# Kernel tuning notes

Measured on AMD Instinct MI355X. Metric: run time of the kernel, lower is better.

The kernel has to match this reference:

```python
import jax, jax.numpy as jnp
import numpy as np

D = 128          # embed_features
N = 4096         # cells per batch
M = 8192         # genes / regions
FB1, FB2, FR, FA = 100, 100, 256, 512


def setup_inputs() -> dict:
    key = jax.random.key(0)
    ks = jax.random.split(key, 16)
    s = 0.05  # weight scale to keep activations in a sane range
    return {
        "u1": jax.random.normal(ks[0], (N, FB1), jnp.float32),
        "u2": jax.random.normal(ks[1], (N, FB2), jnp.float32),
        "v1": jax.random.normal(ks[2], (M, FR), jnp.float32),
        "v2": jax.random.normal(ks[3], (M, FA), jnp.float32),
        # linear layers stored as [in, out] so y = x @ W
        "Wb1": jax.random.normal(ks[4], (FB1, D), jnp.float32) * s,
        "Wb2": jax.random.normal(ks[5], (FB2, D), jnp.float32) * s,
        "Wrna1": jax.random.normal(ks[6], (FR, 2 * D), jnp.float32) * s,
        "Wrna2": jax.random.normal(ks[7], (2 * D, D), jnp.float32) * s,
        "gene_act": jax.random.normal(ks[8], (FA, FR), jnp.float32) * s,
        "w_prod1": jax.random.normal(ks[9], (D,), jnp.float32),
        "w_add1": jax.random.normal(ks[10], (2 * D,), jnp.float32),
        "w_prod2": jax.random.normal(ks[11], (D,), jnp.float32),
        "w_add2": jax.random.normal(ks[12], (2 * D,), jnp.float32),
        "bias_1": jax.random.normal(ks[13], (), jnp.float32),
        "bias_2": jax.random.normal(ks[14], (), jnp.float32),
    }


def _pair_scores(eu, ev, w_prod, w_add, bias):
    # Algebraically identical to the original all-pairs form:
    #   (eu[:,None,:] * ev[None,:,:]) @ w_prod  ==  (eu * w_prod) @ ev.T
    #   cat(eu, ev) @ w_add  ==  eu @ w_add[:D]  +  ev @ w_add[D:]
    prod = (eu * w_prod) @ ev.T                     # [N, M]
    add = (eu @ w_add[:D])[:, None] + (ev @ w_add[D:])[None, :]
    return prod + add + bias                        # [N, M]


def reference(u1, u2, v1, v2, Wb1, Wb2, Wrna1, Wrna2, gene_act,
              w_prod1, w_add1, w_prod2, w_add2, bias_1, bias_2):
    # mode='linear' activations -> identity
    embed_u1 = u1 @ Wb1                                          # [N, D]
    embed_v1 = jax.nn.relu(v1 @ Wrna1) @ Wrna2                   # [M, D]
    out1 = jax.nn.relu(_pair_scores(embed_u1, embed_v1, w_prod1, w_add1, bias_1))

    embed_u2 = u2 @ Wb2                                          # [N, D]
    embed_v2 = jax.nn.relu((v2 @ gene_act) @ Wrna1) @ Wrna2      # [M, D]
    out2 = jax.nn.sigmoid(_pair_scores(embed_u2, embed_v2, w_prod2, w_add2, bias_2))

    return out1, out2, embed_u1, embed_v1, embed_u2, embed_v2
```

## Files before the change

### kernel.cpp

```cpp
#include <hip/hip_runtime.h>
#include <math.h>

#define N_CELLS 4096
#define M_GENES 8192

typedef __attribute__((ext_vector_type(8))) short short8;
typedef __attribute__((ext_vector_type(4))) float f32x4;

__device__ __align__(16) float g_a[24576];

__device__ __align__(16) short g_bu1[N_CELLS * 128];
__device__ __align__(16) short g_bv1[M_GENES * 128];
__device__ __align__(16) short g_bu2[N_CELLS * 128];
__device__ __align__(16) short g_bv2[M_GENES * 128];

__device__ __align__(16) short g_gaT[256 * 512];
__device__ __align__(16) short g_W1T[256 * 256];
__device__ __align__(16) short g_W2T[128 * 256];
__device__ __align__(16) short g_ub1[N_CELLS * 128];
__device__ __align__(16) short g_ub2[N_CELLS * 128];
__device__ __align__(16) short g_WbT1[128 * 128];
__device__ __align__(16) short g_WbT2[128 * 128];


__device__ __forceinline__ short* bf_sel(int s) {
    switch (s) {
        case 0:  return g_bu1;
        case 1:  return g_bv1;
        case 2:  return g_bu2;
        default: return g_bv2;
    }
}

__device__ __forceinline__ const short* wt_sel(int s) {
    switch (s) {
        case 0:  return g_gaT;
        case 1:  return g_W1T;
        default: return g_W2T;
    }
}

__device__ __forceinline__ short f2bf(float f) {
    unsigned u = __builtin_bit_cast(unsigned, f);
    u += 0x7FFFu + ((u >> 16) & 1u);
    return (short)(u >> 16);
}

__device__ __forceinline__ void cvt8(const float* __restrict__ in, short* __restrict__ out) {
    const float4 x0 = *reinterpret_cast<const float4*>(in);
    const float4 x1 = *reinterpret_cast<const float4*>(in + 4);
    short8 o;
    o[0] = f2bf(x0.x); o[1] = f2bf(x0.y); o[2] = f2bf(x0.z); o[3] = f2bf(x0.w);
    o[4] = f2bf(x1.x); o[5] = f2bf(x1.y); o[6] = f2bf(x1.z); o[7] = f2bf(x1.w);
    *reinterpret_cast<short8*>(out) = o;
}

__device__ __forceinline__ void transpose8(const float* __restrict__ in, short* __restrict__ out,
                                           int c, int K, int Nc) {
    const int o0 = c * 8;
    const int ncol = o0 / K;
    const int k0 = o0 % K;
    short8 o;
#pragma unroll
    for (int j = 0; j < 8; ++j) o[j] = f2bf(in[(size_t)(k0 + j) * Nc + ncol]);
    *reinterpret_cast<short8*>(out + o0) = o;
}

__device__ __forceinline__ void stage_A_f32(char* cA, const float* Af, int row0, int k0, int K, int t)
{
    const float* gAf = Af + (size_t)row0 * K + k0;
#pragma unroll
    for (int c = 0; c < 4; ++c) {
        const int idx = c * 256 + t;
        const int row = idx >> 4, sub = idx & 15;
        const int dst = row * 256 + ((sub * 16) ^ ((row & 7) << 4));
        cvt8(gAf + (size_t)row * K + sub * 8, (short*)(cA + dst));
    }
}

__device__ __forceinline__ void stage_B128(char* cB, const short* BT, int col0, int k0, int K, int t)
{
    const char* gB = (const char*)(BT + (size_t)col0 * K + k0);
#pragma unroll
    for (int c = 0; c < 8; ++c) {
        const int idx = c * 256 + t;
        const int row = idx >> 4, sub = idx & 15;
        const int dst = row * 256 + ((sub * 16) ^ ((row & 7) << 4));
        *(short8*)(cB + dst) = *(const short8*)(gB + (size_t)row * (2 * K) + sub * 16);
    }
}

__device__ __forceinline__ void stage_B64(char* cB, const short* BT, int col0, int k0, int K, int t)
{
    const char* gB = (const char*)(BT + (size_t)col0 * K + k0);
#pragma unroll
    for (int c = 0; c < 4; ++c) {
        const int idx = c * 256 + t;
        const int row = idx >> 4, sub = idx & 15;
        const int dst = row * 256 + ((sub * 16) ^ ((row & 7) << 4));
        *(short8*)(cB + dst) = *(const short8*)(gB + (size_t)row * (2 * K) + sub * 16);
    }
}

__device__ __forceinline__ void mfma128(const char* cA, int strideA, int baseA,
                                        const char* cB, f32x4 (&acc)[2][4], int t)
{
    const int l = t & 63, w = t >> 6;
    const int wm = (w >> 1) * 32, wn = (w & 1) * 64;
    const int lr = l & 15, lkb = (l >> 4) * 16;
#pragma unroll
    for (int kk = 0; kk < 4; ++kk) {
        const int kb = kk * 64 + lkb;
        short8 a[2], b4[4];
#pragma unroll
        for (int i = 0; i < 2; ++i) {
            const int rA = wm + i * 16 + lr;
            a[i] = *(const short8*)(cA + rA * strideA + ((baseA + kb) ^ ((rA & 7) << 4)));
        }
#pragma unroll
        for (int jj = 0; jj < 4; ++jj) {
            const int rB = wn + jj * 16 + lr;
            b4[jj] = *(const short8*)(cB + rB * 256 + (kb ^ ((rB & 7) << 4)));
        }
#pragma unroll
        for (int i = 0; i < 2; ++i)
#pragma unroll
            for (int jj = 0; jj < 4; ++jj)
                acc[i][jj] = __builtin_amdgcn_mfma_f32_16x16x32_bf16(a[i], b4[jj], acc[i][jj], 0, 0, 0);
    }
}

__device__ __forceinline__ void mfma64(const char* cA, int strideA, int baseA,
                                       const char* cB, f32x4 (&acc)[4], int t)
{
    const int l = t & 63, w = t >> 6;
    const int wm = w * 16;
    const int lr = l & 15, lkb = (l >> 4) * 16;
#pragma unroll
    for (int kk = 0; kk < 4; ++kk) {
        const int kb = kk * 64 + lkb;
        const int rA = wm + lr;
        const short8 a = *(const short8*)(cA + rA * strideA + ((baseA + kb) ^ ((rA & 7) << 4)));
#pragma unroll
        for (int jj = 0; jj < 4; ++jj) {
            const int rB = jj * 16 + lr;
            const short8 b = *(const short8*)(cB + rB * 256 + (kb ^ ((rB & 7) << 4)));
            acc[jj] = __builtin_amdgcn_mfma_f32_16x16x32_bf16(a, b, acc[jj], 0, 0, 0);
        }
    }
}

__device__ __forceinline__ void acc_to_sH(char* sH, const f32x4 (&acc)[2][4], int ct, bool relu, int t)
{
    const int l = t & 63, w = t >> 6;
    const int wm = (w >> 1) * 32, wn = (w & 1) * 64;
    const int lr = l & 15, r4 = (l >> 4) * 4;
#pragma unroll
    for (int i = 0; i < 2; ++i)
#pragma unroll
        for (int r = 0; r < 4; ++r) {
            const int row = wm + i * 16 + r4 + r;
#pragma unroll
            for (int jj = 0; jj < 4; ++jj) {
                float x = acc[i][jj][r];
                if (relu) x = fmaxf(x, 0.f);
                const int col = ct * 128 + wn + jj * 16 + lr;
                *(short*)(sH + row * 512 + ((col * 2) ^ ((row & 7) << 4))) = f2bf(x);
            }
        }
}

__device__ __forceinline__ void acc2_to_sH(char* sH, const f32x4 (&a4)[4], int ct, bool relu, int t)
{
    const int l = t & 63, w = t >> 6;
    const int lr = l & 15, r4 = (l >> 4) * 4;
#pragma unroll
    for (int r = 0; r < 4; ++r) {
        const int row = w * 16 + r4 + r;
#pragma unroll
        for (int jj = 0; jj < 4; ++jj) {
            float x = a4[jj][r];
            if (relu) x = fmaxf(x, 0.f);
            const int col = ct * 64 + jj * 16 + lr;
            *(short*)(sH + row * 512 + ((col * 2) ^ ((row & 7) << 4))) = f2bf(x);
        }
    }
}

__device__ __forceinline__ void first_layer(const float* Vf, int row0, int KV, int bsel, bool relu,
                                            char* cA, char* cH, int t)
{
    const short* BT = wt_sel(bsel);
    f32x4 accA[2][4] = {}, accB[2][4] = {};
    for (int k0 = 0; k0 < KV; k0 += 128) {
        stage_A_f32(cA, Vf, row0, k0, KV, t);
        stage_B128(cH, BT, 0, k0, KV, t);
        __syncthreads();
        mfma128(cA, 256, 0, cH, accA, t);
        __syncthreads();
        stage_B128(cH, BT, 128, k0, KV, t);
        __syncthreads();
        mfma128(cA, 256, 0, cH, accB, t);
        __syncthreads();
    }
    acc_to_sH(cH, accA, 0, relu, t);
    acc_to_sH(cH, accB, 1, relu, t);
    __syncthreads();
}

__device__ __forceinline__ void mid_layer(char* cH, char* cB64, int t)
{
    const short* W1T = wt_sel(1);
    f32x4 h4[4][4];
#pragma unroll
    for (int ct = 0; ct < 4; ++ct)
#pragma unroll
        for (int jj = 0; jj < 4; ++jj) h4[ct][jj] = (f32x4){0.f, 0.f, 0.f, 0.f};
#pragma unroll
    for (int ct = 0; ct < 4; ++ct)
        for (int k0 = 0; k0 < 2; ++k0) {
            stage_B64(cB64, W1T, ct * 64, k0 * 128, 256, t);
            __syncthreads();
            mfma64(cH, 512, k0 * 256, cB64, h4[ct], t);
            __syncthreads();
        }
#pragma unroll
    for (int ct = 0; ct < 4; ++ct) acc2_to_sH(cH, h4[ct], ct, true, t);
    __syncthreads();
}

__device__ __forceinline__ void final_layer(char* cH, char* cB64, float* evout, short* bv,
                                            const float* w_add_hi, int a_ofs, int row0, int t)
{
    const short* W2T = wt_sel(2);
    const int l = t & 63, w = t >> 6, lr = l & 15, r4 = (l >> 4) * 4;
    float part[4] = {0.f, 0.f, 0.f, 0.f};
#pragma unroll
    for (int ct = 0; ct < 2; ++ct) {
        f32x4 a2[4] = {};
        for (int k0 = 0; k0 < 2; ++k0) {
            stage_B64(cB64, W2T, ct * 64, k0 * 128, 256, t);
            __syncthreads();
            mfma64(cH, 512, k0 * 256, cB64, a2, t);
            __syncthreads();
        }
#pragma unroll
        for (int r = 0; r < 4; ++r) {
            const int grow = row0 + w * 16 + r4 + r;
#pragma unroll
            for (int jj = 0; jj < 4; ++jj) {
                const float x = a2[jj][r];
                const int col = ct * 64 + jj * 16 + lr;
                evout[(size_t)grow * 128 + col] = x;
                bv[(size_t)grow * 128 + col] = f2bf(x);
                part[r] = fmaf(x, w_add_hi[col], part[r]);
            }
        }
    }
#pragma unroll
    for (int off = 1; off < 16; off <<= 1)
#pragma unroll
        for (int r = 0; r < 4; ++r) part[r] += __shfl_xor(part[r], off, 64);
    if (lr == 0) {
#pragma unroll
        for (int r = 0; r < 4; ++r) g_a[a_ofs + row0 + w * 16 + r4 + r] = part[r];
    }
}

__device__ __forceinline__ void embed_mfma(int eb, const float* wp1, const float* wa1,
                                           const float* wp2, const float* wa2,
                                           float* eu1, float* eu2,
                                           char* cA, char* cB64, char* cH, int t)
{
    const int which = eb >> 6;
    const int row0 = (eb & 63) * 64;
    const short* Au  = which ? g_ub2  : g_ub1;
    const short* WbT = which ? g_WbT2 : g_WbT1;
    const float* wp = which ? wp2 : wp1;
    const float* wa = which ? wa2 : wa1;
    float* eu = which ? eu2 : eu1;
    short* bu = bf_sel(which ? 2 : 0);
    const int a_ofs = which ? 12288 : 0;

    stage_B64(cA, Au, row0, 0, 128, t);
    stage_B128(cH, WbT, 0, 0, 128, t);
    __syncthreads();
    f32x4 acc[2][4] = {};
    mfma128(cA, 256, 0, cH, acc, t);
    __syncthreads();

    const int l = t & 63, w = t >> 6;
    const int wm = (w >> 1) * 32, wn = (w & 1) * 64;
    const int lr = l & 15, r4 = (l >> 4) * 4;
    float* sRow = (float*)cB64;
    float wvp[4], wva[4];
#pragma unroll
    for (int jj = 0; jj < 4; ++jj) {
        const int col = wn + jj * 16 + lr;
        wvp[jj] = wp[col];
        wva[jj] = wa[col];
    }
    float part[2][4] = {};
#pragma unroll
    for (int i = 0; i < 2; ++i)
#pragma unroll
        for (int r = 0; r < 4; ++r) {
            const int grow = row0 + wm + i * 16 + r4 + r;
#pragma unroll
            for (int jj = 0; jj < 4; ++jj) {
                const float x = acc[i][jj][r];
                const int col = wn + jj * 16 + lr;
                eu[(size_t)grow * 128 + col] = x;
                bu[(size_t)grow * 128 + col] = f2bf(x * wvp[jj]);
                part[i][r] = fmaf(x, wva[jj], part[i][r]);
            }
        }
#pragma unroll
    for (int off = 1; off < 16; off <<= 1)
#pragma unroll
        for (int i = 0; i < 2; ++i)
#pragma unroll
            for (int r = 0; r < 4; ++r)
                part[i][r] += __shfl_xor(part[i][r], off, 64);
    if (t < 64) sRow[t] = 0.f;
    __syncthreads();
    if (lr == 0) {
#pragma unroll
        for (int i = 0; i < 2; ++i)
#pragma unroll
            for (int r = 0; r < 4; ++r)
                atomicAdd(&sRow[wm + i * 16 + r4 + r], part[i][r]);
    }
    __syncthreads();
    if (t < 64) g_a[a_ofs + row0 + t] = sRow[t];
}

__device__ __forceinline__ void pair_tile(int which, int bb, char* cA, char* cB,
                                          const float* bias1, const float* bias2,
                                          float* out1, float* out2, int t)
{
    const int l = t & 63;
    const int col0 = (bb & 63) * 128;
    const int row0 = (bb >> 6) * 128;
    {
        const short8* gA = reinterpret_cast<const short8*>(bf_sel(which ? 2 : 0)) + (size_t)row0 * 16;
        const short8* gB = reinterpret_cast<const short8*>(bf_sel(which ? 3 : 1)) + (size_t)col0 * 16;
#pragma unroll
        for (int c = 0; c < 8; ++c) {
            const int idx = c * 256 + t;
            const int row = idx >> 4, sub = idx & 15;
            const int dst = row * 256 + ((sub * 16) ^ ((row & 7) << 4));
            const short8 va = gA[idx];
            const short8 vb = gB[idx];
            *(short8*)(cA + dst) = va;
            *(short8*)(cB + dst) = vb;
        }
    }
    __syncthreads();

    const int w  = t >> 6;
    const int wm = (w >> 1) * 64;
    const int wn = (w & 1) * 64;
    const int lr = l & 15;
    const int lkb = (l >> 4) * 16;

    f32x4 acc[4][4] = {};
#pragma unroll
    for (int kk = 0; kk < 4; ++kk) {
        const int kb = kk * 64 + lkb;
        short8 a[4], bfr[4];
#pragma unroll
        for (int i = 0; i < 4; ++i) {
            const int rowA = wm + i * 16 + lr;
            a[i] = *(const short8*)(cA + rowA * 256 + (kb ^ ((rowA & 7) << 4)));
            const int rowB = wn + i * 16 + lr;
            bfr[i] = *(const short8*)(cB + rowB * 256 + (kb ^ ((rowB & 7) << 4)));
        }
#pragma unroll
        for (int i = 0; i < 4; ++i)
#pragma unroll
            for (int jj = 0; jj < 4; ++jj)
                acc[i][jj] = __builtin_amdgcn_mfma_f32_16x16x32_bf16(a[i], bfr[jj], acc[i][jj], 0, 0, 0);
    }

    const float bias = which ? *bias2 : *bias1;
    float* outp = which ? out2 : out1;
    const int ofsU = which ? 12288 : 0;
    const int ofsV = which ? 16384 : 4096;
    const int r4 = (l >> 4) * 4;
    float au[4][4];
#pragma unroll
    for (int i = 0; i < 4; ++i)
#pragma unroll
        for (int r = 0; r < 4; ++r)
            au[i][r] = g_a[ofsU + row0 + wm + i * 16 + r4 + r];
    float av[4];
#pragma unroll
    for (int jj = 0; jj < 4; ++jj)
        av[jj] = g_a[ofsV + col0 + wn + jj * 16 + lr];

#pragma unroll
    for (int i = 0; i < 4; ++i) {
#pragma unroll
        for (int r = 0; r < 4; ++r) {
            const int grow = row0 + wm + i * 16 + r4 + r;
            float* orow = outp + (size_t)grow * M_GENES + col0 + wn;
#pragma unroll
            for (int jj = 0; jj < 4; ++jj) {
                float x = acc[i][jj][r] + au[i][r] + av[jj] + bias;
                if (which == 0) x = fmaxf(x, 0.f);
                else            x = __builtin_amdgcn_rcpf(1.f + __expf(-x));
                orow[jj * 16 + lr] = x;
            }
        }
    }
}

__global__ __launch_bounds__(256) void prep_all2(const float* __restrict__ gene_act,
                                                 const float* __restrict__ W1,
                                                 const float* __restrict__ W2,
                                                 const float* __restrict__ u1,
                                                 const float* __restrict__ u2,
                                                 const float* __restrict__ Wb1,
                                                 const float* __restrict__ Wb2)
{
    const int b = blockIdx.x, t = threadIdx.x;
    if (b < 64)       transpose8(gene_act, g_gaT, b * 256 + t, 512, 256);
    else if (b < 96)  transpose8(W1, g_W1T, (b - 64) * 256 + t, 256, 256);
    else if (b < 112) transpose8(W2, g_W2T, (b - 96) * 256 + t, 256, 128);
    else if (b < 624) {
        const int which = (b >= 368);
        const int c = (b - (which ? 368 : 112)) * 256 + t;
        const float* u = which ? u2 : u1;
        short* ub = which ? g_ub2 : g_ub1;
        const int row = c >> 4, sub = c & 15;
        short8 o = {0, 0, 0, 0, 0, 0, 0, 0};
        if (sub < 12) {
            const float4 x0 = *(const float4*)(u + row * 100 + sub * 8);
            const float4 x1 = *(const float4*)(u + row * 100 + sub * 8 + 4);
            o[0] = f2bf(x0.x); o[1] = f2bf(x0.y); o[2] = f2bf(x0.z); o[3] = f2bf(x0.w);
            o[4] = f2bf(x1.x); o[5] = f2bf(x1.y); o[6] = f2bf(x1.z); o[7] = f2bf(x1.w);
        } else if (sub == 12) {
            const float4 x0 = *(const float4*)(u + row * 100 + 96);
            o[0] = f2bf(x0.x); o[1] = f2bf(x0.y); o[2] = f2bf(x0.z); o[3] = f2bf(x0.w);
        }
        *(short8*)(ub + (size_t)c * 8) = o;
    } else {
        const int which = (b >= 632);
        const int c = (b - (which ? 632 : 624)) * 256 + t;
        const float* Wb = which ? Wb2 : Wb1;
        short* wt = which ? g_WbT2 : g_WbT1;
        const int col = c >> 4, k0 = (c & 15) * 8;
        short8 o;
#pragma unroll
        for (int j = 0; j < 8; ++j)
            o[j] = (k0 + j < 100) ? f2bf(Wb[(size_t)(k0 + j) * 128 + col]) : (short)0;
        *(short8*)(wt + (size_t)c * 8) = o;
    }
}

__global__ __launch_bounds__(256) void fused_s1(const float* __restrict__ v1,
                                                const float* __restrict__ wp1,
                                                const float* __restrict__ wa1,
                                                const float* __restrict__ wp2,
                                                const float* __restrict__ wa2,
                                                float* __restrict__ eu1,
                                                float* __restrict__ eu2,
                                                float* __restrict__ ev1)
{
    __shared__ __align__(16) short sMem[32768];
    char* cA   = (char*)sMem;
    char* cB64 = cA + 16384;
    char* cH   = cA + 32768;
    const int b = blockIdx.x, t = threadIdx.x;
    if (b < 128) {
        const int row0 = b * 64;
        first_layer(v1, row0, 256, 1, true, cA, cH, t);
        final_layer(cH, cB64, ev1, bf_sel(1), wa1 + 128, 4096, row0, t);
    } else {
        embed_mfma(b - 128, wp1, wa1, wp2, wa2, eu1, eu2, cA, cB64, cH, t);
    }
}

__global__ __launch_bounds__(256) void pair1_s2(const float* __restrict__ v2,
                                                const float* __restrict__ wa2,
                                                float* __restrict__ ev2,
                                                const float* __restrict__ bias1,
                                                const float* __restrict__ bias2,
                                                float* __restrict__ out1,
                                                float* __restrict__ out2)
{
    __shared__ __align__(16) short sMem[32768];
    char* cA   = (char*)sMem;
    char* cB64 = cA + 16384;
    char* cH   = cA + 32768;
    const int b = blockIdx.x, t = threadIdx.x;
    if (b < 128) {
        const int row0 = b * 64;
        first_layer(v2, row0, 512, 0, false, cA, cH, t);
        mid_layer(cH, cB64, t);
        final_layer(cH, cB64, ev2, bf_sel(3), wa2 + 128, 16384, row0, t);
    } else {
        pair_tile(0, b - 128, cA, cA + 32768, bias1, bias2, out1, out2, t);
    }
}

__global__ __launch_bounds__(256) void pair2_k(const float* __restrict__ bias1,
                                               const float* __restrict__ bias2,
                                               float* __restrict__ out1,
                                               float* __restrict__ out2)
{
    __shared__ __align__(16) short sMem[32768];
    pair_tile(1, blockIdx.x, (char*)sMem, (char*)sMem + 32768, bias1, bias2,
              out1, out2, threadIdx.x);
}

extern "C" void kernel_launch(void* const* d_in, const int* in_sizes, int n_in,
                              void* d_out, int out_size, void* d_ws, size_t ws_size,
                              hipStream_t stream)
{
    const float* u1       = (const float*)d_in[0];
    const float* u2       = (const float*)d_in[1];
    const float* v1       = (const float*)d_in[2];
    const float* v2       = (const float*)d_in[3];
    const float* Wb1      = (const float*)d_in[4];
    const float* Wb2      = (const float*)d_in[5];
    const float* Wrna1    = (const float*)d_in[6];
    const float* Wrna2    = (const float*)d_in[7];
    const float* gene_act = (const float*)d_in[8];
    const float* w_prod1  = (const float*)d_in[9];
    const float* w_add1   = (const float*)d_in[10];
    const float* w_prod2  = (const float*)d_in[11];
    const float* w_add2   = (const float*)d_in[12];
    const float* bias1    = (const float*)d_in[13];
    const float* bias2    = (const float*)d_in[14];

    float* out  = (float*)d_out;
    float* out1 = out;
    float* out2 = out1 + (size_t)N_CELLS * M_GENES;
    float* eu1  = out2 + (size_t)N_CELLS * M_GENES;
    float* ev1  = eu1 + N_CELLS * 128;
    float* eu2  = ev1 + M_GENES * 128;
    float* ev2  = eu2 + N_CELLS * 128;

    prep_all2<<<640, 256, 0, stream>>>(gene_act, Wrna1, Wrna2, u1, u2, Wb1, Wb2);

    fused_s1<<<256, 256, 0, stream>>>(v1, w_prod1, w_add1, w_prod2, w_add2,
                                      eu1, eu2, ev1);

    pair1_s2<<<2176, 256, 0, stream>>>(v2, w_add2, ev2, bias1, bias2, out1, out2);

    pair2_k<<<2048, 256, 0, stream>>>(bias1, bias2, out1, out2);
}
```

Baseline: 111.2 us.

## Shrink pair-score tiles to 64x64, rebalance kernels, and use nontemporal stores

Pair-score output tiles drop from 128x128 to 64x64, with each wave computing 32x32. The work is redistributed so the first fused kernel handles the v2 embedding plus most of pair1, and a second kernel handles the rest of pair1 plus all of pair2. Output stores switch to nontemporal to avoid cache pollution on the large write stream. The aim is better load balance and overlap with the embedding blocks, at the cost of more operand reloads and smaller MFMA tiles per wave.

```diff
diff --git a/kernel.cpp b/kernel.cpp
--- a/kernel.cpp
+++ b/kernel.cpp
@@ -335,18 +335,18 @@
     if (t < 64) g_a[a_ofs + row0 + t] = sRow[t];
 }
 
-__device__ __forceinline__ void pair_tile(int which, int bb, char* cA, char* cB,
-                                          const float* bias1, const float* bias2,
-                                          float* out1, float* out2, int t)
+__device__ __forceinline__ void pair_tile64(int which, int bb, char* cA, char* cB,
+                                            const float* bias1, const float* bias2,
+                                            float* out1, float* out2, int t)
 {
     const int l = t & 63;
-    const int col0 = (bb & 63) * 128;
-    const int row0 = (bb >> 6) * 128;
+    const int col0 = (bb & 127) * 64;
+    const int row0 = (bb >> 7) * 64;
     {
         const short8* gA = reinterpret_cast<const short8*>(bf_sel(which ? 2 : 0)) + (size_t)row0 * 16;
         const short8* gB = reinterpret_cast<const short8*>(bf_sel(which ? 3 : 1)) + (size_t)col0 * 16;
 #pragma unroll
-        for (int c = 0; c < 8; ++c) {
+        for (int c = 0; c < 4; ++c) {
             const int idx = c * 256 + t;
             const int row = idx >> 4, sub = idx & 15;
             const int dst = row * 256 + ((sub * 16) ^ ((row & 7) << 4));
@@ -359,28 +359,28 @@
     __syncthreads();
 
     const int w  = t >> 6;
-    const int wm = (w >> 1) * 64;
-    const int wn = (w & 1) * 64;
+    const int wm = (w & 1) * 32;
+    const int wn = (w >> 1) * 32;
     const int lr = l & 15;
     const int lkb = (l >> 4) * 16;
 
-    f32x4 acc[4][4] = {};
+    f32x4 acc[2][2] = {};
 #pragma unroll
     for (int kk = 0; kk < 4; ++kk) {
         const int kb = kk * 64 + lkb;
-        short8 a[4], bfr[4];
-#pragma unroll
-        for (int i = 0; i < 4; ++i) {
-            const int rowA = wm + i * 16 + lr;
-            a[i] = *(const short8*)(cA + rowA * 256 + (kb ^ ((rowA & 7) << 4)));
-            const int rowB = wn + i * 16 + lr;
-            bfr[i] = *(const short8*)(cB + rowB * 256 + (kb ^ ((rowB & 7) << 4)));
-        }
-#pragma unroll
-        for (int i = 0; i < 4; ++i)
-#pragma unroll
-            for (int jj = 0; jj < 4; ++jj)
-                acc[i][jj] = __builtin_amdgcn_mfma_f32_16x16x32_bf16(a[i], bfr[jj], acc[i][jj], 0, 0, 0);
+        short8 a[2], b2[2];
+#pragma unroll
+        for (int i = 0; i < 2; ++i) {
+            const int rA = wm + i * 16 + lr;
+            a[i] = *(const short8*)(cA + rA * 256 + (kb ^ ((rA & 7) << 4)));
+            const int rB = wn + i * 16 + lr;
+            b2[i] = *(const short8*)(cB + rB * 256 + (kb ^ ((rB & 7) << 4)));
+        }
+#pragma unroll
+        for (int i = 0; i < 2; ++i)
+#pragma unroll
+            for (int j = 0; j < 2; ++j)
+                acc[i][j] = __builtin_amdgcn_mfma_f32_16x16x32_bf16(a[i], b2[j], acc[i][j], 0, 0, 0);
     }
 
     const float bias = which ? *bias2 : *bias1;
@@ -388,29 +388,29 @@
     const int ofsU = which ? 12288 : 0;
     const int ofsV = which ? 16384 : 4096;
     const int r4 = (l >> 4) * 4;
-    float au[4][4];
-#pragma unroll
-    for (int i = 0; i < 4; ++i)
+    float au[2][4];
+#pragma unroll
+    for (int i = 0; i < 2; ++i)
 #pragma unroll
         for (int r = 0; r < 4; ++r)
             au[i][r] = g_a[ofsU + row0 + wm + i * 16 + r4 + r];
-    float av[4];
-#pragma unroll
-    for (int jj = 0; jj < 4; ++jj)
-        av[jj] = g_a[ofsV + col0 + wn + jj * 16 + lr];
-
-#pragma unroll
-    for (int i = 0; i < 4; ++i) {
+    float av[2];
+#pragma unroll
+    for (int j = 0; j < 2; ++j)
+        av[j] = g_a[ofsV + col0 + wn + j * 16 + lr];
+
+#pragma unroll
+    for (int i = 0; i < 2; ++i) {
 #pragma unroll
         for (int r = 0; r < 4; ++r) {
             const int grow = row0 + wm + i * 16 + r4 + r;
             float* orow = outp + (size_t)grow * M_GENES + col0 + wn;
 #pragma unroll
-            for (int jj = 0; jj < 4; ++jj) {
-                float x = acc[i][jj][r] + au[i][r] + av[jj] + bias;
+            for (int j = 0; j < 2; ++j) {
+                float x = acc[i][j][r] + au[i][r] + av[j] + bias;
                 if (which == 0) x = fmaxf(x, 0.f);
                 else            x = __builtin_amdgcn_rcpf(1.f + __expf(-x));
-                orow[jj * 16 + lr] = x;
+                __builtin_nontemporal_store(x, orow + j * 16 + lr);
             }
         }
     }
@@ -501,18 +501,23 @@
         mid_layer(cH, cB64, t);
         final_layer(cH, cB64, ev2, bf_sel(3), wa2 + 128, 16384, row0, t);
     } else {
-        pair_tile(0, b - 128, cA, cA + 32768, bias1, bias2, out1, out2, t);
-    }
-}
-
-__global__ __launch_bounds__(256) void pair2_k(const float* __restrict__ bias1,
-                                               const float* __restrict__ bias2,
-                                               float* __restrict__ out1,
-                                               float* __restrict__ out2)
-{
-    __shared__ __align__(16) short sMem[32768];
-    pair_tile(1, blockIdx.x, (char*)sMem, (char*)sMem + 32768, bias1, bias2,
-              out1, out2, threadIdx.x);
+        pair_tile64(0, b - 128, cA, cA + 16384, bias1, bias2, out1, out2, t);
+    }
+}
+
+__global__ __launch_bounds__(256) void pair_rest(const float* __restrict__ bias1,
+                                                 const float* __restrict__ bias2,
+                                                 float* __restrict__ out1,
+                                                 float* __restrict__ out2)
+{
+    __shared__ __align__(16) short sMem[16384];
+    const int b = blockIdx.x;
+    if (b < 2048)
+        pair_tile64(0, b + 6144, (char*)sMem, (char*)sMem + 16384, bias1, bias2,
+                    out1, out2, threadIdx.x);
+    else
+        pair_tile64(1, b - 2048, (char*)sMem, (char*)sMem + 16384, bias1, bias2,
+                    out1, out2, threadIdx.x);
 }
 
 extern "C" void kernel_launch(void* const* d_in, const int* in_sizes, int n_in,
@@ -548,7 +553,7 @@
     fused_s1<<<256, 256, 0, stream>>>(v1, w_prod1, w_add1, w_prod2, w_add2,
                                       eu1, eu2, ev1);
 
-    pair1_s2<<<2176, 256, 0, stream>>>(v2, w_add2, ev2, bias1, bias2, out1, out2);
-
-    pair2_k<<<2048, 256, 0, stream>>>(bias1, bias2, out1, out2);
-}
+    pair1_s2<<<6272, 256, 0, stream>>>(v2, w_add2, ev2, bias1, bias2, out1, out2);
+
+    pair_rest<<<10240, 256, 0, stream>>>(bias1, bias2, out1, out2);
+}
```

New measurement: 102.3 us (median of 2 runs). 1.09x faster.
